# Performance work log

Hardware: AMD Instinct MI355X
Metric: run time of the kernel (lower is better)

Reference implementation:

```python
import jax, jax.numpy as jnp
import numpy as np

INVALID_CLS = tuple(range(240, 256))
TEMPERATURE = 1.0
PRED_PER_IM = 100
B, Q, C = 256, 900, 256


def setup_inputs() -> dict:
    key = jax.random.key(0)
    k1, k2, k3, k4 = jax.random.split(key, 4)
    pred_logits = jax.random.normal(k1, (B, Q, C), dtype=jnp.float32)
    pred_obj = jax.random.uniform(k2, (B, Q), dtype=jnp.float32)
    pred_boxes = jax.random.uniform(k3, (B, Q, 4), dtype=jnp.float32)
    # target sizes ~ realistic image resolutions (h, w)
    target_sizes = jax.random.uniform(k4, (B, 2), dtype=jnp.float32) * 800.0 + 200.0
    return {"pred_logits": pred_logits, "pred_obj": pred_obj,
            "pred_boxes": pred_boxes, "target_sizes": target_sizes}


def _cxcywh_to_xyxy(boxes):
    cx, cy, w, h = jnp.split(boxes, 4, axis=-1)
    return jnp.concatenate([cx - 0.5 * w, cy - 0.5 * h,
                            cx + 0.5 * w, cy + 0.5 * h], axis=-1)


def reference(pred_logits, pred_obj, pred_boxes, target_sizes):
    b, q, c = pred_logits.shape
    invalid = jnp.array(INVALID_CLS)
    logits = pred_logits.at[:, :, invalid].set(-1e11)
    # fused probability: exp(-T * energy) * sigmoid(logits)
    obj_prob = jnp.exp(-TEMPERATURE * pred_obj)[..., None]          # [B,Q,1]
    fused = obj_prob * jax.nn.sigmoid(logits)                       # [B,Q,C]
    scores, topk_idx = jax.lax.top_k(fused.reshape(b, q * c), PRED_PER_IM)
    topk_boxes = topk_idx // c                                      # [B,K]
    labels = topk_idx % c                                           # [B,K]
    boxes_xyxy = _cxcywh_to_xyxy(pred_boxes)                        # [B,Q,4]
    gather_idx = jnp.broadcast_to(topk_boxes[:, :, None], (b, PRED_PER_IM, 4))
    boxes = jnp.take_along_axis(boxes_xyxy, gather_idx, axis=1)     # [B,K,4]
    img_h, img_w = target_sizes[:, 0], target_sizes[:, 1]
    scale = jnp.stack([img_w, img_h, img_w, img_h], axis=1)         # [B,4]
    boxes = boxes * scale[:, None, :]
    return scores, labels, boxes
```

## Files before the change

kernel.cpp:

```cpp
#include <hip/hip_runtime.h>
#include <stdint.h>

#define NB 256
#define NQ 900
#define NC 256
#define TOPK 100
#define QC (NQ * NC)
#define NBINS_S 4096
#define CAP 4096
#define FCAP 512
#define KS 25
#define SHIFT 18


__device__ inline float fastsig(float x) {
    return __builtin_amdgcn_rcpf(1.0f + __expf(-x));
}

__global__ __launch_bounds__(1024)
void postproc_kernel(const float* __restrict__ logits,
                     const float* __restrict__ obj,
                     const float* __restrict__ pboxes,
                     const float* __restrict__ tsz,
                     float* __restrict__ out)
{
    const int b = blockIdx.x;
    const int tid = threadIdx.x;
    const int wid = tid >> 6;
    const int lane = tid & 63;

    __shared__ unsigned int pool[NBINS_S];
    __shared__ float eobj[NQ];
    __shared__ unsigned int cbits[CAP];
    __shared__ int cidx[CAP];
    __shared__ int activeQ[NQ];
    __shared__ unsigned int part[1024];
    __shared__ unsigned int part2[32];
    __shared__ int s_thrBin, s_cnt, s_nActive, s_c2;
    __shared__ int s_dig, s_above, s_nfin;

    unsigned int* shist = pool;

    for (int i = tid; i < NBINS_S; i += 1024) shist[i] = 0;
    if (tid == 0) { s_cnt = 0; s_nActive = 0; }
    if (tid < NQ) eobj[tid] = expf(-obj[b * NQ + tid]);
    __syncthreads();

    const float4* lg4 = (const float4*)(logits + (size_t)b * QC);

    for (int j = wid; j < 56; j += 16) {
        int q = j * 16 + 8;
        if (lane < 60) {
            float eo = eobj[q];
            float4 v = lg4[(q << 6) + lane];
            float s0 = eo * fastsig(v.x);
            float s1 = eo * fastsig(v.y);
            float s2 = eo * fastsig(v.z);
            float s3 = eo * fastsig(v.w);
            atomicAdd(&shist[__float_as_uint(s0) >> SHIFT], 1u);
            atomicAdd(&shist[__float_as_uint(s1) >> SHIFT], 1u);
            atomicAdd(&shist[__float_as_uint(s2) >> SHIFT], 1u);
            atomicAdd(&shist[__float_as_uint(s3) >> SHIFT], 1u);
        }
    }
    __syncthreads();

    {
        unsigned int sum = 0;
        #pragma unroll
        for (int j = 0; j < 4; ++j) sum += shist[tid * 4 + j];
        part[tid] = sum;
    }
    __syncthreads();
    if (tid < 32) {
        unsigned int s2 = 0;
        #pragma unroll
        for (int j = 0; j < 32; ++j) s2 += part[tid * 32 + j];
        part2[tid] = s2;
    }
    __syncthreads();
    if (tid == 0) {
        int cum = 0;
        int sc = 31;
        while (sc > 0 && cum + (int)part2[sc] < KS) { cum += (int)part2[sc]; --sc; }
        int pc = sc * 32 + 31, plo = sc * 32;
        while (pc > plo && cum + (int)part[pc] < KS) { cum += (int)part[pc]; --pc; }
        int bin = pc * 4 + 3, blo = pc * 4;
        while (bin > blo && cum + (int)shist[bin] < KS) { cum += (int)shist[bin]; --bin; }
        s_thrBin = bin;
    }
    __syncthreads();
    unsigned int thrBits = (unsigned int)s_thrBin << SHIFT;

    if (tid < NQ) {
        if (__float_as_uint(eobj[tid]) >= thrBits) {
            int p = atomicAdd(&s_nActive, 1);
            activeQ[p] = tid;
        }
    }
    __syncthreads();
    const int nA = s_nActive;

    for (int j = wid; j < nA; j += 16) {
        int q = activeQ[j];
        if (lane < 60) {
            float eo = eobj[q];
            float4 v = lg4[(q << 6) + lane];
            #pragma unroll
            for (int j2 = 0; j2 < 4; ++j2) {
                float x = (j2 == 0) ? v.x : (j2 == 1) ? v.y : (j2 == 2) ? v.z : v.w;
                float s = eo * (1.0f / (1.0f + expf(-x)));
                unsigned int bits = __float_as_uint(s);
                if (bits >= thrBits) {
                    int p = atomicAdd(&s_cnt, 1);
                    if (p < CAP) {
                        cbits[p] = bits;
                        cidx[p] = (q << 8) + (lane << 2) + j2;
                    }
                }
            }
        }
    }
    __syncthreads();
    int M = s_cnt;

    if (M < TOPK || M > CAP) {
        int lo = 0, hi = NBINS_S - 1;
        while (lo < hi) {
            int mid = (lo + hi + 1) >> 1;
            unsigned int tb = (unsigned int)mid << SHIFT;
            if (tid == 0) s_c2 = 0;
            __syncthreads();
            int local = 0;
            for (int j = wid; j < NQ; j += 16) {
                if (__float_as_uint(eobj[j]) >= tb && lane < 60) {
                    float eo = eobj[j];
                    float4 v = lg4[(j << 6) + lane];
                    local += (__float_as_uint(eo * (1.0f / (1.0f + expf(-v.x)))) >= tb);
                    local += (__float_as_uint(eo * (1.0f / (1.0f + expf(-v.y)))) >= tb);
                    local += (__float_as_uint(eo * (1.0f / (1.0f + expf(-v.z)))) >= tb);
                    local += (__float_as_uint(eo * (1.0f / (1.0f + expf(-v.w)))) >= tb);
                }
            }
            atomicAdd(&s_c2, local);
            __syncthreads();
            if (s_c2 >= TOPK) lo = mid; else hi = mid - 1;
            __syncthreads();
        }
        unsigned int tb = (unsigned int)lo << SHIFT;
        thrBits = tb;
        if (tid == 0) s_cnt = 0;
        __syncthreads();
        for (int j = wid; j < NQ; j += 16) {
            if (__float_as_uint(eobj[j]) >= tb && lane < 60) {
                float eo = eobj[j];
                float4 v = lg4[(j << 6) + lane];
                #pragma unroll
                for (int j2 = 0; j2 < 4; ++j2) {
                    float x = (j2 == 0) ? v.x : (j2 == 1) ? v.y : (j2 == 2) ? v.z : v.w;
                    float s = eo * (1.0f / (1.0f + expf(-x)));
                    unsigned int bits = __float_as_uint(s);
                    if (bits >= tb) {
                        int p = atomicAdd(&s_cnt, 1);
                        if (p < CAP) {
                            cbits[p] = bits;
                            cidx[p] = (j << 8) + (lane << 2) + j2;
                        }
                    }
                }
            }
        }
        __syncthreads();
        M = s_cnt;
    }
    M = min(M, CAP);

    unsigned int* rhist = part;
    unsigned int* rsuf  = part + 256;
    unsigned int prefixVal = 0;
    int need = TOPK;
    int startShift = 24;
    if ((thrBits >> 24) == 0x3Fu) { prefixVal = 0x3F000000u; startShift = 16; }
    for (int shift = startShift; shift >= 0; shift -= 8) {
        if (tid < 256) rhist[tid] = 0;
        __syncthreads();
        unsigned int pmask = (shift >= 24) ? 0u : (0xFFFFFFFFu << (shift + 8));
        for (int i = tid; i < M; i += 1024) {
            unsigned int bb = cbits[i];
            if ((bb & pmask) == (prefixVal & pmask))
                atomicAdd(&rhist[(bb >> shift) & 255], 1u);
        }
        __syncthreads();
        if (tid < 64) {
            unsigned int h0 = rhist[tid * 4 + 0];
            unsigned int h1 = rhist[tid * 4 + 1];
            unsigned int h2 = rhist[tid * 4 + 2];
            unsigned int h3 = rhist[tid * 4 + 3];
            unsigned int loc = h0 + h1 + h2 + h3;
            unsigned int suf = loc;
            #pragma unroll
            for (int d = 1; d < 64; d <<= 1) {
                unsigned int o = __shfl_down(suf, d);
                suf += (tid + d < 64) ? o : 0u;
            }
            unsigned int above = suf - loc;
            rsuf[tid * 4 + 3] = above + h3;
            rsuf[tid * 4 + 2] = above + h3 + h2;
            rsuf[tid * 4 + 1] = above + h3 + h2 + h1;
            rsuf[tid * 4 + 0] = above + h3 + h2 + h1 + h0;
        }
        __syncthreads();
        if (tid < 256) {
            int sv = (int)rsuf[tid];
            int sa = (tid == 255) ? 0 : (int)rsuf[tid + 1];
            if (sv >= need && sa < need) { s_dig = tid; s_above = sa; }
        }
        __syncthreads();
        prefixVal |= ((unsigned int)s_dig) << shift;
        need -= s_above;
    }
    const unsigned int kth = prefixVal;

    unsigned int* fb = pool;
    int* fi = (int*)(pool + FCAP);
    if (tid == 0) s_nfin = 0;
    __syncthreads();
    for (int i = tid; i < M; i += 1024) {
        unsigned int bb = cbits[i];
        if (bb >= kth) {
            int p = atomicAdd(&s_nfin, 1);
            if (p < FCAP) { fb[p] = bb; fi[p] = cidx[i]; }
        }
    }
    __syncthreads();
    const int n = min(s_nfin, FCAP);

    const float ih = tsz[b * 2 + 0];
    const float iw = tsz[b * 2 + 1];
    float* out_scores = out;
    float* out_labels = out + NB * TOPK;
    float* out_boxes  = out + 2 * NB * TOPK;

    for (int i = tid; i < n; i += 1024) {
        unsigned int mb = fb[i];
        int mi = fi[i];
        int rank = 0;
        for (int j = 0; j < n; ++j) {
            unsigned int ob = fb[j];
            int oi = fi[j];
            rank += (ob > mb) || (ob == mb && oi < mi);
        }
        if (rank < TOPK) {
            int q = mi >> 8;
            int c = mi & 255;
            out_scores[b * TOPK + rank] = __uint_as_float(mb);
            out_labels[b * TOPK + rank] = (float)c;
            const float* bp = pboxes + ((size_t)b * NQ + q) * 4;
            float cx = bp[0], cy = bp[1], w = bp[2], h = bp[3];
            float* dst = out_boxes + ((size_t)b * TOPK + rank) * 4;
            dst[0] = (cx - 0.5f * w) * iw;
            dst[1] = (cy - 0.5f * h) * ih;
            dst[2] = (cx + 0.5f * w) * iw;
            dst[3] = (cy + 0.5f * h) * ih;
        }
    }
}

extern "C" void kernel_launch(void* const* d_in, const int* in_sizes, int n_in,
                              void* d_out, int out_size, void* d_ws, size_t ws_size,
                              hipStream_t stream) {
    const float* logits = (const float*)d_in[0];
    const float* obj    = (const float*)d_in[1];
    const float* boxes  = (const float*)d_in[2];
    const float* tsz    = (const float*)d_in[3];
    float* out = (float*)d_out;
    hipLaunchKernelGGL(postproc_kernel, dim3(NB), dim3(1024), 0, stream,
                       logits, obj, boxes, tsz, out);
}
```

Before: 37.77 us.

## Split single kernel into three launches to parallelize candidate collection across blocks

```diff
diff --git a/kernel.cpp b/kernel.cpp
--- a/kernel.cpp
+++ b/kernel.cpp
@@ -8,42 +8,45 @@
 #define QC (NQ * NC)
 #define NBINS_S 4096
 #define CAP 4096
+#define BCAP 2048
 #define FCAP 512
 #define KS 25
 #define SHIFT 18
 
-
-__device__ inline float fastsig(float x) {
+#define W_THR   0
+#define W_NACT  256
+#define W_CCNT  512
+#define W_OVF   768
+#define W_EOBJ  1024
+#define W_AQ    (W_EOBJ + NB * NQ)
+#define W_CAND  (W_AQ + NB * NQ)
+
+__device__ __forceinline__ float fastsig(float x) {
     return __builtin_amdgcn_rcpf(1.0f + __expf(-x));
 }
 
 __global__ __launch_bounds__(1024)
-void postproc_kernel(const float* __restrict__ logits,
-                     const float* __restrict__ obj,
-                     const float* __restrict__ pboxes,
-                     const float* __restrict__ tsz,
-                     float* __restrict__ out)
+void kA(const float* __restrict__ obj, const float* __restrict__ logits,
+        unsigned* __restrict__ wsu, float* __restrict__ wsf)
 {
     const int b = blockIdx.x;
     const int tid = threadIdx.x;
     const int wid = tid >> 6;
     const int lane = tid & 63;
 
-    __shared__ unsigned int pool[NBINS_S];
+    __shared__ unsigned shist[NBINS_S];
     __shared__ float eobj[NQ];
-    __shared__ unsigned int cbits[CAP];
-    __shared__ int cidx[CAP];
-    __shared__ int activeQ[NQ];
-    __shared__ unsigned int part[1024];
-    __shared__ unsigned int part2[32];
-    __shared__ int s_thrBin, s_cnt, s_nActive, s_c2;
-    __shared__ int s_dig, s_above, s_nfin;
-
-    unsigned int* shist = pool;
-
+    __shared__ unsigned part[1024];
+    __shared__ unsigned part2[32];
+    __shared__ int s_thrBin, s_nActive;
+
+    if (tid == 0) { wsu[W_CCNT + b] = 0u; wsu[W_OVF + b] = 0u; s_nActive = 0; }
     for (int i = tid; i < NBINS_S; i += 1024) shist[i] = 0;
-    if (tid == 0) { s_cnt = 0; s_nActive = 0; }
-    if (tid < NQ) eobj[tid] = expf(-obj[b * NQ + tid]);
+    for (int i = tid; i < NQ; i += 1024) {
+        float e = expf(-obj[b * NQ + i]);
+        eobj[i] = e;
+        wsf[W_EOBJ + b * NQ + i] = e;
+    }
     __syncthreads();
 
     const float4* lg4 = (const float4*)(logits + (size_t)b * QC);
@@ -53,27 +56,23 @@
         if (lane < 60) {
             float eo = eobj[q];
             float4 v = lg4[(q << 6) + lane];
-            float s0 = eo * fastsig(v.x);
-            float s1 = eo * fastsig(v.y);
-            float s2 = eo * fastsig(v.z);
-            float s3 = eo * fastsig(v.w);
-            atomicAdd(&shist[__float_as_uint(s0) >> SHIFT], 1u);
-            atomicAdd(&shist[__float_as_uint(s1) >> SHIFT], 1u);
-            atomicAdd(&shist[__float_as_uint(s2) >> SHIFT], 1u);
-            atomicAdd(&shist[__float_as_uint(s3) >> SHIFT], 1u);
+            atomicAdd(&shist[__float_as_uint(eo * fastsig(v.x)) >> SHIFT], 1u);
+            atomicAdd(&shist[__float_as_uint(eo * fastsig(v.y)) >> SHIFT], 1u);
+            atomicAdd(&shist[__float_as_uint(eo * fastsig(v.z)) >> SHIFT], 1u);
+            atomicAdd(&shist[__float_as_uint(eo * fastsig(v.w)) >> SHIFT], 1u);
         }
     }
     __syncthreads();
 
     {
-        unsigned int sum = 0;
+        unsigned sum = 0;
         #pragma unroll
         for (int j = 0; j < 4; ++j) sum += shist[tid * 4 + j];
         part[tid] = sum;
     }
     __syncthreads();
     if (tid < 32) {
-        unsigned int s2 = 0;
+        unsigned s2 = 0;
         #pragma unroll
         for (int j = 0; j < 32; ++j) s2 += part[tid * 32 + j];
         part2[tid] = s2;
@@ -90,45 +89,114 @@
         s_thrBin = bin;
     }
     __syncthreads();
-    unsigned int thrBits = (unsigned int)s_thrBin << SHIFT;
-
-    if (tid < NQ) {
-        if (__float_as_uint(eobj[tid]) >= thrBits) {
-            int p = atomicAdd(&s_nActive, 1);
-            activeQ[p] = tid;
-        }
-    }
-    __syncthreads();
-    const int nA = s_nActive;
-
-    for (int j = wid; j < nA; j += 16) {
-        int q = activeQ[j];
-        if (lane < 60) {
-            float eo = eobj[q];
-            float4 v = lg4[(q << 6) + lane];
-            #pragma unroll
-            for (int j2 = 0; j2 < 4; ++j2) {
-                float x = (j2 == 0) ? v.x : (j2 == 1) ? v.y : (j2 == 2) ? v.z : v.w;
-                float s = eo * (1.0f / (1.0f + expf(-x)));
-                unsigned int bits = __float_as_uint(s);
-                if (bits >= thrBits) {
-                    int p = atomicAdd(&s_cnt, 1);
-                    if (p < CAP) {
-                        cbits[p] = bits;
-                        cidx[p] = (q << 8) + (lane << 2) + j2;
-                    }
-                }
+    const unsigned thrBits = (unsigned)s_thrBin << SHIFT;
+    if (tid == 0) wsu[W_THR + b] = thrBits;
+
+    if (tid < NQ && __float_as_uint(eobj[tid]) >= thrBits) {
+        int p = atomicAdd(&s_nActive, 1);
+        wsu[W_AQ + b * NQ + p] = (unsigned)tid;
+    }
+    __syncthreads();
+    if (tid == 0) wsu[W_NACT + b] = (unsigned)s_nActive;
+}
+
+__global__ __launch_bounds__(256)
+void kB(const float* __restrict__ logits, unsigned* __restrict__ wsu,
+        const float* __restrict__ wsf)
+{
+    const int blk = blockIdx.x;
+    const int b = blk >> 2;
+    const int s = blk & 3;
+    const int tid = threadIdx.x;
+    const int w = tid >> 6;
+    const int lane = tid & 63;
+
+    __shared__ int2 stage[BCAP];
+    __shared__ int s_local, s_base;
+
+    if (tid == 0) s_local = 0;
+    __syncthreads();
+
+    const unsigned thrBits = wsu[W_THR + b];
+    const int nA = (int)wsu[W_NACT + b];
+    const float4* lg4 = (const float4*)(logits + (size_t)b * QC);
+    const int g = s * 4 + w;
+
+    for (int j = g; j < nA; j += 16) {
+        int q = (int)wsu[W_AQ + b * NQ + j];
+        float eo = wsf[W_EOBJ + b * NQ + q];
+        float4 v = make_float4(0.f, 0.f, 0.f, 0.f);
+        bool ok = (lane < 60);
+        if (ok) v = lg4[(q << 6) + lane];
+        #pragma unroll
+        for (int j2 = 0; j2 < 4; ++j2) {
+            float x = (j2 == 0) ? v.x : (j2 == 1) ? v.y : (j2 == 2) ? v.z : v.w;
+            float sc = eo * (1.0f / (1.0f + expf(-x)));
+            unsigned bits = __float_as_uint(sc);
+            if (ok && bits >= thrBits) {
+                int p = atomicAdd(&s_local, 1);
+                if (p < BCAP) stage[p] = make_int2((int)bits, (q << 8) + (lane << 2) + j2);
             }
         }
     }
     __syncthreads();
-    int M = s_cnt;
-
-    if (M < TOPK || M > CAP) {
+
+    const int loc = s_local;
+    const int put = min(loc, BCAP);
+    if (tid == 0) {
+        s_base = (int)atomicAdd(&wsu[W_CCNT + b], (unsigned)put);
+        if (loc > BCAP) atomicOr(&wsu[W_OVF + b], 1u);
+    }
+    __syncthreads();
+    const int base = s_base;
+    int2* cand = (int2*)(wsu + W_CAND);
+    for (int i = tid; i < put; i += 256) {
+        int p = base + i;
+        if (p < CAP) cand[b * CAP + p] = stage[i];
+    }
+}
+
+__global__ __launch_bounds__(1024)
+void kC(const float* __restrict__ logits, const float* __restrict__ pboxes,
+        const float* __restrict__ tsz, float* __restrict__ out,
+        unsigned* __restrict__ wsu, const float* __restrict__ wsf)
+{
+    const int b = blockIdx.x;
+    const int tid = threadIdx.x;
+    const int wid = tid >> 6;
+    const int lane = tid & 63;
+
+    __shared__ unsigned cbits[CAP];
+    __shared__ int cidx[CAP];
+    __shared__ float eobj[NQ];
+    __shared__ unsigned rhist[256], rsuf[256];
+    __shared__ unsigned fbv[FCAP];
+    __shared__ int fiv[FCAP];
+    __shared__ int s_cnt, s_c2, s_dig, s_above, s_nfin;
+
+    unsigned thrBits = wsu[W_THR + b];
+    const int Mraw = (int)wsu[W_CCNT + b];
+    const int ovf = (int)wsu[W_OVF + b];
+    const float4* lg4 = (const float4*)(logits + (size_t)b * QC);
+    const int2* cand = (const int2*)(wsu + W_CAND);
+    int M;
+
+    if (Mraw >= TOPK && Mraw <= CAP && !ovf) {
+        M = Mraw;
+        for (int i = tid; i < M; i += 1024) {
+            int2 cc = cand[b * CAP + i];
+            cbits[i] = (unsigned)cc.x;
+            cidx[i] = cc.y;
+        }
+        __syncthreads();
+    } else {
+        for (int i = tid; i < NQ; i += 1024) eobj[i] = wsf[W_EOBJ + b * NQ + i];
+        if (tid == 0) s_cnt = 0;
+        __syncthreads();
         int lo = 0, hi = NBINS_S - 1;
         while (lo < hi) {
             int mid = (lo + hi + 1) >> 1;
-            unsigned int tb = (unsigned int)mid << SHIFT;
+            unsigned tb = (unsigned)mid << SHIFT;
             if (tid == 0) s_c2 = 0;
             __syncthreads();
             int local = 0;
@@ -147,9 +215,8 @@
             if (s_c2 >= TOPK) lo = mid; else hi = mid - 1;
             __syncthreads();
         }
-        unsigned int tb = (unsigned int)lo << SHIFT;
+        unsigned tb = (unsigned)lo << SHIFT;
         thrBits = tb;
-        if (tid == 0) s_cnt = 0;
         __syncthreads();
         for (int j = wid; j < NQ; j += 16) {
             if (__float_as_uint(eobj[j]) >= tb && lane < 60) {
@@ -158,52 +225,46 @@
                 #pragma unroll
                 for (int j2 = 0; j2 < 4; ++j2) {
                     float x = (j2 == 0) ? v.x : (j2 == 1) ? v.y : (j2 == 2) ? v.z : v.w;
-                    float s = eo * (1.0f / (1.0f + expf(-x)));
-                    unsigned int bits = __float_as_uint(s);
+                    float sc = eo * (1.0f / (1.0f + expf(-x)));
+                    unsigned bits = __float_as_uint(sc);
                     if (bits >= tb) {
                         int p = atomicAdd(&s_cnt, 1);
-                        if (p < CAP) {
-                            cbits[p] = bits;
-                            cidx[p] = (j << 8) + (lane << 2) + j2;
-                        }
+                        if (p < CAP) { cbits[p] = bits; cidx[p] = (j << 8) + (lane << 2) + j2; }
                     }
                 }
             }
         }
         __syncthreads();
-        M = s_cnt;
-    }
-    M = min(M, CAP);
-
-    unsigned int* rhist = part;
-    unsigned int* rsuf  = part + 256;
-    unsigned int prefixVal = 0;
+        M = min(s_cnt, CAP);
+    }
+
+    unsigned prefixVal = 0;
     int need = TOPK;
     int startShift = 24;
     if ((thrBits >> 24) == 0x3Fu) { prefixVal = 0x3F000000u; startShift = 16; }
     for (int shift = startShift; shift >= 0; shift -= 8) {
         if (tid < 256) rhist[tid] = 0;
         __syncthreads();
-        unsigned int pmask = (shift >= 24) ? 0u : (0xFFFFFFFFu << (shift + 8));
+        unsigned pmask = (shift >= 24) ? 0u : (0xFFFFFFFFu << (shift + 8));
         for (int i = tid; i < M; i += 1024) {
-            unsigned int bb = cbits[i];
+            unsigned bb = cbits[i];
             if ((bb & pmask) == (prefixVal & pmask))
                 atomicAdd(&rhist[(bb >> shift) & 255], 1u);
         }
         __syncthreads();
         if (tid < 64) {
-            unsigned int h0 = rhist[tid * 4 + 0];
-            unsigned int h1 = rhist[tid * 4 + 1];
-            unsigned int h2 = rhist[tid * 4 + 2];
-            unsigned int h3 = rhist[tid * 4 + 3];
-            unsigned int loc = h0 + h1 + h2 + h3;
-            unsigned int suf = loc;
+            unsigned h0 = rhist[tid * 4 + 0];
+            unsigned h1 = rhist[tid * 4 + 1];
+            unsigned h2 = rhist[tid * 4 + 2];
+            unsigned h3 = rhist[tid * 4 + 3];
+            unsigned loc = h0 + h1 + h2 + h3;
+            unsigned suf = loc;
             #pragma unroll
             for (int d = 1; d < 64; d <<= 1) {
-                unsigned int o = __shfl_down(suf, d);
+                unsigned o = __shfl_down(suf, d);
                 suf += (tid + d < 64) ? o : 0u;
             }
-            unsigned int above = suf - loc;
+            unsigned above = suf - loc;
             rsuf[tid * 4 + 3] = above + h3;
             rsuf[tid * 4 + 2] = above + h3 + h2;
             rsuf[tid * 4 + 1] = above + h3 + h2 + h1;
@@ -216,20 +277,18 @@
             if (sv >= need && sa < need) { s_dig = tid; s_above = sa; }
         }
         __syncthreads();
-        prefixVal |= ((unsigned int)s_dig) << shift;
+        prefixVal |= ((unsigned)s_dig) << shift;
         need -= s_above;
     }
-    const unsigned int kth = prefixVal;
-
-    unsigned int* fb = pool;
-    int* fi = (int*)(pool + FCAP);
+    const unsigned kth = prefixVal;
+
     if (tid == 0) s_nfin = 0;
     __syncthreads();
     for (int i = tid; i < M; i += 1024) {
-        unsigned int bb = cbits[i];
+        unsigned bb = cbits[i];
         if (bb >= kth) {
             int p = atomicAdd(&s_nfin, 1);
-            if (p < FCAP) { fb[p] = bb; fi[p] = cidx[i]; }
+            if (p < FCAP) { fbv[p] = bb; fiv[p] = cidx[i]; }
         }
     }
     __syncthreads();
@@ -242,12 +301,12 @@
     float* out_boxes  = out + 2 * NB * TOPK;
 
     for (int i = tid; i < n; i += 1024) {
-        unsigned int mb = fb[i];
-        int mi = fi[i];
+        unsigned mb = fbv[i];
+        int mi = fiv[i];
         int rank = 0;
         for (int j = 0; j < n; ++j) {
-            unsigned int ob = fb[j];
-            int oi = fi[j];
+            unsigned ob = fbv[j];
+            int oi = fiv[j];
             rank += (ob > mb) || (ob == mb && oi < mi);
         }
         if (rank < TOPK) {
@@ -274,6 +333,11 @@
     const float* boxes  = (const float*)d_in[2];
     const float* tsz    = (const float*)d_in[3];
     float* out = (float*)d_out;
-    hipLaunchKernelGGL(postproc_kernel, dim3(NB), dim3(1024), 0, stream,
-                       logits, obj, boxes, tsz, out);
-}
+    unsigned* wsu = (unsigned*)d_ws;
+    float* wsf = (float*)d_ws;
+
+    hipLaunchKernelGGL(kA, dim3(NB), dim3(1024), 0, stream, obj, logits, wsu, wsf);
+    hipLaunchKernelGGL(kB, dim3(NB * 4), dim3(256), 0, stream, logits, wsu, wsf);
+    hipLaunchKernelGGL(kC, dim3(NB), dim3(1024), 0, stream,
+                       logits, boxes, tsz, out, wsu, wsf);
+}
```

After: 46.57 us. 23.3% more time.
